# Kernel optimization log

Measured on AMD Instinct MI355X. Metric: run time of the kernel, lower is better.

The kernel has to match this reference:

```python
import jax, jax.numpy as jnp
import numpy as np

EPS = 1e-7
INF = 1e8
SOFT_CENTER_RADIUS = 3.0
TOPK = 13
IOU_WEIGHT = 3.0
NUM_CLASSES = 80
N_PRIORS = 33600
NUM_GT = 256
IMG = 1024.0


def setup_inputs() -> dict:
    key = jax.random.key(0)
    k1, k2, k3, k4, k5, k6, k7 = jax.random.split(key, 7)
    n, g, c = N_PRIORS, NUM_GT, NUM_CLASSES
    pred_scores = jax.random.normal(k1, (n, c), jnp.float32)
    # priors: (cx, cy, stride, stride)
    ctr = jax.random.uniform(k2, (n, 2), jnp.float32) * IMG
    stride = jnp.full((n, 1), 8.0, jnp.float32)
    priors = jnp.concatenate([ctr, stride, stride], axis=-1)
    # predicted boxes, x1y1x2y2
    pwh = jax.random.uniform(k3, (n, 2), jnp.float32) * 96.0 + 8.0
    pctr = jax.random.uniform(k4, (n, 2), jnp.float32) * IMG
    pred_bboxes = jnp.concatenate([pctr - pwh / 2, pctr + pwh / 2], axis=-1)
    # gt boxes, x1y1x2y2
    gwh = jax.random.uniform(k5, (g, 2), jnp.float32) * 192.0 + 16.0
    gctr = jax.random.uniform(k6, (g, 2), jnp.float32) * IMG
    gt_bboxes = jnp.concatenate([gctr - gwh / 2, gctr + gwh / 2], axis=-1)
    gt_labels = jax.random.randint(k7, (g,), 0, c, dtype=jnp.int32).astype(jnp.int64)
    return {"pred_scores": pred_scores, "priors": priors,
            "pred_bboxes": pred_bboxes, "gt_bboxes": gt_bboxes,
            "gt_labels": gt_labels}


def _pairwise_iou(a, b):
    # a: (n,4), b: (g,4), x1y1x2y2 -> (n,g)
    area_a = (a[:, 2] - a[:, 0]) * (a[:, 3] - a[:, 1])
    area_b = (b[:, 2] - b[:, 0]) * (b[:, 3] - b[:, 1])
    lt = jnp.maximum(a[:, None, :2], b[None, :, :2])
    rb = jnp.minimum(a[:, None, 2:], b[None, :, 2:])
    wh = jnp.clip(rb - lt, 0.0, None)
    inter = wh[..., 0] * wh[..., 1]
    union = area_a[:, None] + area_b[None, :] - inter
    return inter / jnp.maximum(union, 1e-6)


def reference(pred_scores, priors, pred_bboxes, gt_bboxes, gt_labels):
    n, g = pred_bboxes.shape[0], gt_bboxes.shape[0]
    gt_labels = gt_labels.astype(jnp.int32)

    # ---- find_inside_points (box_dim == 4) ----
    pts = priors[:, :2]                                   # (n,2)
    lt = pts[:, None, :] - gt_bboxes[None, :, :2]
    rb = gt_bboxes[None, :, 2:] - pts[:, None, :]
    is_in_gts = jnp.min(jnp.concatenate([lt, rb], -1), -1) > 0   # (n,g)
    pad_bbox_flag = gt_bboxes.sum(-1) > 0                        # (g,)
    is_in_gts = is_in_gts & pad_bbox_flag[None, :]
    valid_mask = jnp.any(is_in_gts, -1)                          # (n,)

    # ---- soft center prior ----
    gt_center = (gt_bboxes[:, :2] + gt_bboxes[:, 2:]) * 0.5      # (g,2)
    dist = jnp.sqrt(((pts[:, None, :] - gt_center[None, :, :]) ** 2).sum(-1))
    dist = dist / priors[:, 2:3]                                 # / stride
    dist = dist * valid_mask[:, None].astype(dist.dtype)
    soft_center_prior = jnp.power(10.0, dist - SOFT_CENTER_RADIUS)

    # ---- iou cost ----
    ious = _pairwise_iou(pred_bboxes, gt_bboxes)                 # (n,g)
    iou_cost = -jnp.log(ious + EPS) * IOU_WEIGHT

    # ---- soft classification cost (BCE-with-logits, iou targets) ----
    logits = pred_scores[:, gt_labels]                           # (n,g)
    scale = jnp.abs(ious - jax.nn.sigmoid(logits)) ** 2
    bce = jnp.maximum(logits, 0) - logits * ious + jnp.log1p(jnp.exp(-jnp.abs(logits)))
    cost = bce * scale + iou_cost + soft_center_prior
    cost = jnp.where(valid_mask[:, None], cost, INF)

    # ---- dynamic k matching (vectorized over GTs) ----
    K = min(TOPK, n)
    topk_ious, _ = jax.lax.top_k(ious.T, K)                      # (g,K)
    dynamic_ks = jnp.clip(topk_ious.sum(-1).astype(jnp.int32), 1, None)  # (g,)
    _, cand_idx = jax.lax.top_k(-cost.T, K)                      # (g,K) lowest-cost priors per gt
    sel = (jnp.arange(K)[None, :] < dynamic_ks[:, None]).astype(jnp.float32)
    matching = jnp.zeros((g, n), jnp.float32).at[
        jnp.arange(g)[:, None], cand_idx].set(sel).T             # (n,g)

    # resolve priors matched to multiple gts -> keep min-cost gt
    multi = matching.sum(-1) > 1
    onehot_min = jax.nn.one_hot(jnp.argmin(cost, -1), g, dtype=jnp.float32)
    matching = jnp.where(multi[:, None], onehot_min, matching)

    fg = matching.sum(-1) > 0
    matched_gt_inds = jnp.argmax(matching, -1)                   # (n,)
    matched_pred_ious = (matching * ious).sum(-1)                # (n,)

    final = fg & valid_mask
    assigned_gt_inds = jnp.where(final, matched_gt_inds + 1, 0)
    assigned_labels = jnp.where(final, gt_labels[matched_gt_inds], -1)
    max_overlaps = jnp.where(final, matched_pred_ious, -INF)
    return assigned_gt_inds, max_overlaps, assigned_labels
```

## Files before the change

kernel.cpp:

```cpp
#include <hip/hip_runtime.h>
#include <cstdint>

#define NPRI 33600
#define NGT  256
#define NCLS 80
#define KTOP 13
#define INF_F 1.0e8f
#define EPS_F 1e-7f
#define L10 3.3219280948873623f
#define SCN_T 512
#define NW   (SCN_T / 64)
#define CAPI 4096
#define CAPC 1024
#define RFIX 5.5f
#define NBX  32
#define NB   (NBX * NBX)
#define PREP_BLKS ((NPRI + 255) / 256)
#define NEGINF __int_as_float(0xff800000)

typedef unsigned long long u64;

__device__ __forceinline__ int get_label(const void* p, int j, int is64) {
    if (is64) return (int)((const long long*)p)[j];
    return ((const int*)p)[j];
}

__device__ __forceinline__ int bin1(float c) {
    int b = (int)floorf(c * 0.03125f);
    return b < 0 ? 0 : (b > NBX - 1 ? NBX - 1 : b);
}

__device__ __forceinline__ float wave_max_bc_f32(float v) {
    #pragma unroll
    for (int off = 32; off > 0; off >>= 1) v = fmaxf(v, __shfl_down(v, off, 64));
    return __int_as_float(__builtin_amdgcn_readfirstlane(__float_as_int(v)));
}
__device__ __forceinline__ u64 wave_min_bc_u64(u64 v) {
    #pragma unroll
    for (int off = 32; off > 0; off >>= 1) { u64 o = __shfl_down(v, off, 64); v = (o < v) ? o : v; }
    unsigned lo = (unsigned)__builtin_amdgcn_readfirstlane((int)(v & 0xffffffffull));
    unsigned hi = (unsigned)__builtin_amdgcn_readfirstlane((int)(v >> 32));
    return (((u64)hi) << 32) | lo;
}
// ... 23 lines not shown
        if (lane == 0) dst[r] = bm;
    }
}

__device__ __forceinline__ float iou_exact(float4 pb, float areap, float gx1, float gy1,
                                           float gx2, float gy2, float areag) {
    float iw = fmaxf(fminf(pb.z, gx2) - fmaxf(pb.x, gx1), 0.0f);
    float ih = fmaxf(fminf(pb.w, gy2) - fmaxf(pb.y, gy1), 0.0f);
    float inter = iw * ih;
    return inter / fmaxf(areap + areag - inter, 1e-6f);
}
__device__ __forceinline__ float cost_exact(float4 p2, float gcx, float gcy,
                                            float l, float iou) {
    float dx = p2.x - gcx, dy = p2.y - gcy;
    float dist = sqrtf(dx * dx + dy * dy) / p2.z;
    float soft = exp2f((dist - 3.0f) * L10);
    float sig = 1.0f / (1.0f + expf(-l));
    float dd = iou - sig;
    float bce = fmaxf(l, 0.0f) - l * iou + log1pf(expf(-fabsf(l)));
    float iouc = -logf(iou + EPS_F) * 3.0f;
    return bce * (dd * dd) + iouc + soft;
}

__global__ __launch_bounds__(256) void k_prep(
        const float* __restrict__ priors, const float* __restrict__ gt,
        const void* labels, const float* __restrict__ pboxes,
        float4* __restrict__ pbp,
        int* count, int* firstgt, int* flag,
        int* histI, int* histC, int* maxbuf) {
    __shared__ float4 gbox[NGT];
    __shared__ int    gpad[NGT];
    __shared__ int    bad;
    __shared__ int    lhI[NB];
    __shared__ int    lhC[NB];
    __shared__ int    lmax0, lmax1;
    const int tid = threadIdx.x;
    const int b = blockIdx.x;
    if (b == 0 && tid == 0) bad = 0;
    if (tid == 0) { lmax0 = 0; lmax1 = 0; }
    for (int t = tid; t < NB; t += 256) { lhI[t] = 0; lhC[t] = 0; }
    {
        float4 bx = ((const float4*)gt)[tid];
        gbox[tid] = bx;
        gpad[tid] = ((bx.x + bx.y + bx.z + bx.w) > 0.0f) ? 1 : 0;
    }
    __syncthreads();
    if (b == 0 && tid < 128) {
        long long v = ((const long long*)labels)[tid];
        if (v < 0 || v >= NCLS) atomicOr(&bad, 1);
    }
    int g = b * 256 + tid;
    if (g < NPRI) {
        count[g] = 0; firstgt[g] = NGT;
        float4 pr = ((const float4*)priors)[g];
        float px = pr.x, py = pr.y;
        int v = 0;
        for (int j = 0; j < NGT; ++j) {
            float4 bx = gbox[j];
            float m = fminf(fminf(px - bx.x, py - bx.y), fminf(bx.z - px, bx.w - py));
            if (m > 0.0f && gpad[j]) { v = 1; break; }
        }
        float rad = pr.z * RFIX;
        float w = v ? rad * rad * (1.0f + 1e-5f) : -1.0f;
        float4 pb = ((const float4*)pboxes)[g];
        pbp[2 * g]     = pb;
        pbp[2 * g + 1] = make_float4(px, py, pr.z, w);
        float pcx = (pb.x + pb.z) * 0.5f, pcy = (pb.y + pb.w) * 0.5f;
        atomicAdd(&lhI[bin1(pcy) * NBX + bin1(pcx)], 1);
        atomicAdd(&lhC[bin1(py) * NBX + bin1(px)], 1);
        float hw = fmaxf((pb.z - pb.x) * 0.5f, 0.0f);
        float hh = fmaxf((pb.w - pb.y) * 0.5f, 0.0f);
        atomicMax(&lmax0, __float_as_int(fmaxf(hw, hh)));
        if (v) atomicMax(&lmax1, __float_as_int(w));
    }
    __syncthreads();
    for (int t = tid; t < NB; t += 256) {
        int h = lhI[t]; if (h) atomicAdd(&histI[t], h);
        h = lhC[t];     if (h) atomicAdd(&histC[t], h);
    }
    if (tid == 0) {
        atomicMax(&maxbuf[0], lmax0);
        atomicMax(&maxbuf[1], lmax1);
    }
    if (b == 0) {
        if (tid == 0) *flag = bad ? 0 : 1;
    }
}

__global__ __launch_bounds__(NB) void k_bins(
        const int* __restrict__ histI, const int* __restrict__ histC,
        int* startI, int* startC, int* curI, int* curC) {
    __shared__ int sc[NB];
    const int t = threadIdx.x;
    int h = histI[t];
    sc[t] = h;
    __syncthreads();
    for (int off = 1; off < NB; off <<= 1) {
        int u = (t >= off) ? sc[t - off] : 0;
        __syncthreads();
        sc[t] += u;
        __syncthreads();
    }
    int excl = sc[t] - h;
    startI[t] = excl; curI[t] = excl;
    if (t == NB - 1) startI[NB] = sc[t];
    __syncthreads();
    h = histC[t];
    sc[t] = h;
    __syncthreads();
    for (int off = 1; off < NB; off <<= 1) {
        int u = (t >= off) ? sc[t - off] : 0;
        __syncthreads();
        sc[t] += u;
        __syncthreads();
    }
    excl = sc[t] - h;
    startC[t] = excl; curC[t] = excl;
    if (t == NB - 1) startC[NB] = sc[t];
}

__global__ __launch_bounds__(256) void k_scatter(
        const float4* __restrict__ pbp,
        int* curI, int* curC,
        float4* __restrict__ A_pb, float4* __restrict__ A_pc) {
    const int i = blockIdx.x * 256 + threadIdx.x;
    if (i >= NPRI) return;
    float4 pb = pbp[2 * i];
    float4 p2 = pbp[2 * i + 1];
    float pcx = (pb.x + pb.z) * 0.5f, pcy = (pb.y + pb.w) * 0.5f;
    int r = atomicAdd(&curI[bin1(pcy) * NBX + bin1(pcx)], 1);
    A_pb[r] = pb;
    int r2 = atomicAdd(&curC[bin1(p2.y) * NBX + bin1(p2.x)], 1);
    A_pc[r2] = make_float4(p2.x, p2.y, p2.w, __int_as_float(i));
}

__global__ __launch_bounds__(SCN_T) void k_scan(
        const float* __restrict__ scores,
        const float4* __restrict__ pbp,
        const float4* __restrict__ A_pb, const float4* __restrict__ A_pc,
        const int* __restrict__ startI, const int* __restrict__ startC,
        const int* __restrict__ maxbuf,
        const float* __restrict__ gt, const void* labels, const int* flag,
        int* count, int* firstgt) {
    const int tid = threadIdx.x, lane = tid & 63, wid = tid >> 6;
    const int j = blockIdx.x;
    const int is64 = *flag;

    const float4 gb = ((const float4*)gt)[j];
    const float gx1 = gb.x, gy1 = gb.y, gx2 = gb.z, gy2 = gb.w;
    const float areag = (gx2 - gx1) * (gy2 - gy1);
    const float gcx = (gx1 + gx2) * 0.5f, gcy = (gy1 + gy2) * 0.5f;
    const int lab = get_label(labels, j, is64);
    const float hmax = __int_as_float(maxbuf[0]);
    const float wmax = __int_as_float(maxbuf[1]);
    const float M = 2.0f * hmax + 1.0f;
    const float rmax = sqrtf(fmaxf(wmax, 0.0f)) + 1.0f;

    __shared__ int s_ni, s_nc, s_mode;
    __shared__ float s_dmax;
    __shared__ float liou[CAPI];
    __shared__ int lcost[CAPC];
    __shared__ float wiof[(NW - 1) * KTOP];
    __shared__ u64 wco[NW * KTOP];
    __shared__ u64 csel[KTOP];
    __shared__ float s_iou13[KTOP];
    if (tid == 0) { s_ni = 0; s_nc = 0; }
    __syncthreads();

    {
        int lox = bin1(gx1 - M), hix = bin1(gx2 + M);
        int loy = bin1(gy1 - M), hiy = bin1(gy2 + M);
        for (int by = loy; by <= hiy; ++by) {
            int s0 = startI[by * NBX + lox];
            int e0 = startI[by * NBX + hix + 1];
            for (int r = s0 + tid; r < e0; r += SCN_T) {
                float4 pb = A_pb[r];
                float areap = (pb.z - pb.x) * (pb.w - pb.y);
                float iou = iou_exact(pb, areap, gx1, gy1, gx2, gy2, areag);
                if (iou > 0.0f) {
                    int p = atomicAdd(&s_ni, 1);
                    if (p < CAPI) liou[p] = iou;
                }
            }
        }
    }
    {
        int lox = bin1(gcx - rmax), hix = bin1(gcx + rmax);
        int loy = bin1(gcy - rmax), hiy = bin1(gcy + rmax);
        for (int by = loy; by <= hiy; ++by) {
            int s0 = startC[by * NBX + lox];
            int e0 = startC[by * NBX + hix + 1];
            for (int r = s0 + tid; r < e0; r += SCN_T) {
                float4 pc = A_pc[r];
                float dx = pc.x - gcx, dy = pc.y - gcy;
                if (dx * dx + dy * dy <= pc.z) {
                    int p = atomicAdd(&s_nc, 1);
                    if (p < CAPC) lcost[p] = __float_as_int(pc.w);
                }
            }
        }
    }
    __syncthreads();
    const int ni = s_ni, nc = s_nc;
    const int ncc = (nc < CAPC) ? nc : CAPC;
    const bool fI = (ni > CAPI);

    if (wid == 0) {
        u64 lf[KTOP];
        #pragma unroll
        for (int s = 0; s < KTOP; ++s) lf[s] = ~0ull;
        for (int k = lane; k < ncc; k += 64) {
            int i = lcost[k];
            float4 pb = pbp[2 * i];
            float4 p2 = pbp[2 * i + 1];
            float areap = (pb.z - pb.x) * (pb.w - pb.y);
            float iou = iou_exact(pb, areap, gx1, gy1, gx2, gy2, areag);
            float ec = cost_exact(p2, gcx, gcy, scores[(size_t)i * NCLS + lab], iou);
            u64 ck = (((u64)__float_as_uint(ec)) << 32) | (unsigned)i;
            if (ck < lf[KTOP - 1]) {
                lf[KTOP - 1] = ck;
                #pragma unroll
                for (int s = KTOP - 1; s > 0; --s)
                    if (lf[s] < lf[s - 1]) { u64 t = lf[s]; lf[s] = lf[s - 1]; lf[s - 1] = t; }
            }
        }
        wave_merge_minN<KTOP>(lf, csel, lane);
        if (lane == 0) {
            u64 tk = csel[KTOP - 1];
            int mode; float dmax = 0.0f;
            if (tk == ~0ull) mode = 2;
            else {
                float tau = __uint_as_float((unsigned)(tk >> 32));
                if (!(tau < 9.0e7f)) mode = 2;
                else {
                    dmax = 3.0f + __log2f(tau + 1e-5f) * (1.0f / L10) + 4e-3f;
                    mode = (dmax > RFIX || nc > CAPC) ? 1 : 0;
                }
            }
            s_mode = mode; s_dmax = dmax;
        }
    } else if (!fI) {
        float lf[KTOP];
        #pragma unroll
        for (int s = 0; s < KTOP; ++s) lf[s] = NEGINF;
        int nn = (ni < CAPI) ? ni : CAPI;
        for (int k = (wid - 1) * 64 + lane; k < nn; k += 64 * (NW - 1)) {
            float v = liou[k];
            if (v > lf[0]) {
                lf[0] = v;
                #pragma unroll
                for (int s = 0; s < KTOP - 1; ++s)
                    if (lf[s] > lf[s + 1]) { float t = lf[s]; lf[s] = lf[s + 1]; lf[s + 1] = t; }
            }
        }
        wave_merge_max13_f32<KTOP>(lf, &wiof[(wid - 1) * KTOP], lane);
    }
    __syncthreads();

    if (fI) {
        if (wid > 0) {
            float lf[KTOP];
            #pragma unroll
            for (int s = 0; s < KTOP; ++s) lf[s] = NEGINF;
            for (int i = (wid - 1) * 64 + lane; i < NPRI; i += 64 * (NW - 1)) {
                float4 pb = pbp[2 * i];
                float areap = (pb.z - pb.x) * (pb.w - pb.y);
                float iou = iou_exact(pb, areap, gx1, gy1, gx2, gy2, areag);
                if (iou > 0.0f && iou > lf[0]) {
                    lf[0] = iou;
                    #pragma unroll
                    for (int s = 0; s < KTOP - 1; ++s)
                        if (lf[s] > lf[s + 1]) { float t = lf[s]; lf[s] = lf[s + 1]; lf[s + 1] = t; }
                }
            }
            wave_merge_max13_f32<KTOP>(lf, &wiof[(wid - 1) * KTOP], lane);
        }
        __syncthreads();
    }

    if (wid == 0) {
        int p = 0;
        for (int r = 0; r < KTOP; ++r) {
            float cur = (lane < NW - 1 && p < KTOP) ? wiof[lane * KTOP + p] : NEGINF;
            float bm = wave_max_bc_f32(cur);
            u64 m = __ballot(cur == bm && bm != NEGINF);
            int first = __ffsll(m) - 1;
            if (lane == first) p++;
            if (lane == 0) s_iou13[r] = bm;
        }
    }

    int mode = s_mode;
    if (mode == 1) {
        const float dmax = s_dmax;
        if (tid == 0) s_nc = 0;
        __syncthreads();
        for (int i = tid; i < NPRI; i += SCN_T) {
            float4 p2 = pbp[2 * i + 1];
            if (p2.w > 0.0f) {
                float dx = p2.x - gcx, dy = p2.y - gcy;
                float rad = p2.z * dmax;
                if (dx * dx + dy * dy <= rad * rad * (1.0f + 1e-5f)) {
                    int p = atomicAdd(&s_nc, 1);
                    if (p < CAPC) lcost[p] = i;
                }
            }
        }
        __syncthreads();
        int nc2 = s_nc;
        if (nc2 <= CAPC) {
            if (wid == 0) {
                u64 lf[KTOP];
                #pragma unroll
                for (int s = 0; s < KTOP; ++s) lf[s] = ~0ull;
                for (int k = lane; k < nc2; k += 64) {
                    int i = lcost[k];
                    float4 pb = pbp[2 * i];
                    float4 p2 = pbp[2 * i + 1];
                    float areap = (pb.z - pb.x) * (pb.w - pb.y);
                    float iou = iou_exact(pb, areap, gx1, gy1, gx2, gy2, areag);
                    float ec = cost_exact(p2, gcx, gcy, scores[(size_t)i * NCLS + lab], iou);
                    u64 ck = (((u64)__float_as_uint(ec)) << 32) | (unsigned)i;
                    if (ck < lf[KTOP - 1]) {
                        lf[KTOP - 1] = ck;
                        #pragma unroll
                        for (int s = KTOP - 1; s > 0; --s)
                            if (lf[s] < lf[s - 1]) { u64 t = lf[s]; lf[s] = lf[s - 1]; lf[s - 1] = t; }
                    }
                }
                wave_merge_minN<KTOP>(lf, csel, lane);
            }
        } else {
            mode = 2;
        }
        __syncthreads();
    }
    if (mode == 2) {
        u64 lf[KTOP];
        #pragma unroll
        for (int s = 0; s < KTOP; ++s) lf[s] = ~0ull;
        for (int i = tid; i < NPRI; i += SCN_T) {
            float4 pb = pbp[2 * i];
            float4 p2 = pbp[2 * i + 1];
            float areap = (pb.z - pb.x) * (pb.w - pb.y);
            float iou = iou_exact(pb, areap, gx1, gy1, gx2, gy2, areag);
            float ec = INF_F;
            if (p2.w > 0.0f) ec = cost_exact(p2, gcx, gcy, scores[(size_t)i * NCLS + lab], iou);
            u64 k2 = (((u64)__float_as_uint(ec)) << 32) | (unsigned)i;
            if (k2 < lf[KTOP - 1]) {
                lf[KTOP - 1] = k2;
                #pragma unroll
                for (int s = KTOP - 1; s > 0; --s)
                    if (lf[s] < lf[s - 1]) { u64 t = lf[s]; lf[s] = lf[s - 1]; lf[s - 1] = t; }
            }
        }
        wave_merge_minN<KTOP>(lf, &wco[wid * KTOP], lane);
        __syncthreads();
        if (wid == 0) {
            int p = 0;
            for (int r = 0; r < KTOP; ++r) {
                u64 cur = (lane < NW && p < KTOP) ? wco[lane * KTOP + p] : ~0ull;
                u64 bm = wave_min_bc_u64(cur);
                if (cur == bm && bm != ~0ull) p++;
                if (lane == 0) csel[r] = bm;
            }
        }
        __syncthreads();
    }

    __syncthreads();
    if (wid == 0) {
        float tsum = 0.0f;
        #pragma unroll
        for (int r = 0; r < KTOP; ++r) {
            float v = s_iou13[r];
            tsum += (v == NEGINF) ? 0.0f : v;
        }
        int ks = (int)tsum;
        if (ks < 1) ks = 1;
        if (lane < KTOP && lane < ks) {
            u64 mine = csel[lane];
            if (mine != ~0ull) {
                int idx = (int)(unsigned)(mine & 0xFFFFFFFFull);
                atomicAdd(&count[idx], 1);
                atomicMin(&firstgt[idx], j);
            }
        }
    }
}

__global__ __launch_bounds__(256) void k_assign(
        const float* __restrict__ scores,
        const float4* __restrict__ pbp, const float* __restrict__ gt,
        const void* labels, const int* flag,
        const int* __restrict__ count, const int* __restrict__ firstgt,
        float* __restrict__ out) {
    __shared__ float4 gbox[NGT];
    __shared__ int glab[NGT];
    __shared__ float gcxs[NGT], gcys[NGT], gareas[NGT];
    __shared__ int s_nm;
    __shared__ int s_mlist[256];
    __shared__ u64 red4[4];
    const int tid = threadIdx.x;
    const int is64 = *flag;
    {
        float4 b = ((const float4*)gt)[tid];
        gbox[tid] = b;
        glab[tid] = get_label(labels, tid, is64);
        gcxs[tid] = (b.x + b.z) * 0.5f;
        gcys[tid] = (b.y + b.w) * 0.5f;
        gareas[tid] = (b.z - b.x) * (b.w - b.y);
    }
    if (tid == 0) s_nm = 0;
    __syncthreads();
    const int i = blockIdx.x * 256 + tid;
    const bool act = (i < NPRI);
    if (act) {
        float4 p2 = pbp[2 * i + 1];
        int v = (p2.w > 0.0f) ? 1 : 0;
        int c = count[i];
        float o0 = 0.0f, o1 = -INF_F, o2 = -1.0f;
        if (v && c == 1) {
            int j = firstgt[i];
            float4 pb = pbp[2 * i];
            float areap = (pb.z - pb.x) * (pb.w - pb.y);
            float4 g = gbox[j];
            float iw = fmaxf(fminf(pb.z, g.z) - fmaxf(pb.x, g.x), 0.0f);
            float ih = fmaxf(fminf(pb.w, g.w) - fmaxf(pb.y, g.y), 0.0f);
            float inter = iw * ih;
            float iou = inter / fmaxf(areap + gareas[j] - inter, 1e-6f);
            o0 = (float)(j + 1); o1 = iou; o2 = (float)glab[j];
        } else if (v && c > 1) {
            int p = atomicAdd(&s_nm, 1);
            s_mlist[p] = i;
        }
        out[i] = o0;
        out[NPRI + i] = o1;
        out[2 * NPRI + i] = o2;
    }
    __syncthreads();
    const int nm = s_nm;
    const int j = tid;
    for (int m = 0; m < nm; ++m) {
        const int ii = s_mlist[m];
        float4 pb = pbp[2 * ii];
        float4 p2 = pbp[2 * ii + 1];
        float areap = (pb.z - pb.x) * (pb.w - pb.y);

        float4 g = gbox[j];
        float iw = fmaxf(fminf(pb.z, g.z) - fmaxf(pb.x, g.x), 0.0f);
        float ih = fmaxf(fminf(pb.w, g.w) - fmaxf(pb.y, g.y), 0.0f);
        float inter = iw * ih;
        float iou = inter / fmaxf(areap + gareas[j] - inter, 1e-6f);
        float dx = p2.x - gcxs[j], dy = p2.y - gcys[j];
        float dist = sqrtf(dx * dx + dy * dy) / p2.z;
        float soft = exp2f((dist - 3.0f) * L10);
        float l = scores[(size_t)ii * NCLS + glab[j]];
        float sig = 1.0f / (1.0f + expf(-l));
        float dd = iou - sig;
        float bce = fmaxf(l, 0.0f) - l * iou + log1pf(expf(-fabsf(l)));
        float cost = bce * (dd * dd) + (-logf(iou + EPS_F) * 3.0f) + soft;

        u64 key = (((u64)__float_as_uint(cost)) << 32) | (unsigned)j;
        u64 v = key;
        #pragma unroll
        for (int off = 32; off > 0; off >>= 1) {
            u64 o = __shfl_down(v, off, 64);
            v = (o < v) ? o : v;
        }
        if ((tid & 63) == 0) red4[tid >> 6] = v;
        __syncthreads();
        u64 best = red4[0];
        #pragma unroll
        for (int q = 1; q < 4; ++q) best = (red4[q] < best) ? red4[q] : best;
        if (key == best) {
            out[ii] = (float)(j + 1);
            out[NPRI + ii] = iou;
            out[2 * NPRI + ii] = (float)glab[j];
        }
        __syncthreads();
    }
}

extern "C" void kernel_launch(void* const* d_in, const int* in_sizes, int n_in,
                              void* d_out, int out_size, void* d_ws, size_t ws_size,
                              hipStream_t stream) {
    const float* scores = (const float*)d_in[0];
    const float* priors = (const float*)d_in[1];
    const float* pboxes = (const float*)d_in[2];
    const float* gt     = (const float*)d_in[3];
    const void*  labels = d_in[4];
    float* out = (float*)d_out;

    char* ws = (char*)d_ws;
    size_t off = 0;
    auto alloc = [&](size_t bytes) { size_t o = off; off = (off + bytes + 255) & ~(size_t)255; return o; };
    int*    flag    = (int*)(ws + alloc(4));
    int*    count   = (int*)(ws + alloc((size_t)NPRI * 4));
    int*    firstgt = (int*)(ws + alloc((size_t)NPRI * 4));
    int*    histI   = (int*)(ws + alloc((size_t)(2 * NB + 2) * 4));
    int*    histC   = histI + NB;
    int*    maxbuf  = histI + 2 * NB;
    int*    startI  = (int*)(ws + alloc((size_t)(NB + 1) * 4));
    int*    startC  = (int*)(ws + alloc((size_t)(NB + 1) * 4));
    int*    curI    = (int*)(ws + alloc((size_t)NB * 4));
    int*    curC    = (int*)(ws + alloc((size_t)NB * 4));
    float4* pbp     = (float4*)(ws + alloc((size_t)NPRI * 32));
    float4* A_pb    = (float4*)(ws + alloc((size_t)NPRI * 16));
    float4* A_pc    = (float4*)(ws + alloc((size_t)NPRI * 16));
    (void)ws_size;

    hipMemsetAsync(histI, 0, (size_t)(2 * NB + 2) * 4, stream);
    hipLaunchKernelGGL(k_prep, dim3(PREP_BLKS), dim3(256), 0, stream,
                       priors, gt, labels, pboxes, pbp, count, firstgt, flag,
                       histI, histC, maxbuf);
    hipLaunchKernelGGL(k_bins, dim3(1), dim3(NB), 0, stream,
                       histI, histC, startI, startC, curI, curC);
    hipLaunchKernelGGL(k_scatter, dim3(PREP_BLKS), dim3(256), 0, stream,
                       pbp, curI, curC, A_pb, A_pc);
    hipLaunchKernelGGL(k_scan, dim3(NGT), dim3(SCN_T), 0, stream,
                       scores, pbp, A_pb, A_pc, startI, startC, maxbuf,
                       gt, labels, flag, count, firstgt);
    hipLaunchKernelGGL(k_assign, dim3((NPRI + 255) / 256), dim3(256), 0, stream,
                       scores, pbp, gt, labels, flag, count, firstgt, out);
}
```

Before: 157.0 us.

## Fuse five-kernel pipeline into one cooperative kernel with grid syncs

Replaces the prep, bin-prefix, scatter, per-GT scan and assign kernels with a single cooperative kernel of 256 blocks of 512 threads, separated by grid.sync barriers. The inside-GT test is now done wave-wide with a ballot across 256 GT boxes instead of a serial loop per thread. This removes four kernel launch gaps. In exchange every phase runs on only 256 blocks, and the grid barriers plus higher shared memory use per block could limit occupancy.

```diff
diff --git a/kernel.cpp b/kernel.cpp
--- a/kernel.cpp
+++ b/kernel.cpp
@@ -1,4 +1,5 @@
 #include <hip/hip_runtime.h>
+#include <hip/hip_cooperative_groups.h>
 #include <cstdint>
 
 #define NPRI 33600
@@ -15,10 +16,10 @@
 #define RFIX 5.5f
 #define NBX  32
 #define NB   (NBX * NBX)
-#define PREP_BLKS ((NPRI + 255) / 256)
 #define NEGINF __int_as_float(0xff800000)
 
 typedef unsigned long long u64;
+namespace cg = cooperative_groups;
 
 __device__ __forceinline__ int get_label(const void* p, int j, int is64) {
     if (is64) return (int)((const long long*)p)[j];
@@ -88,140 +89,25 @@
     return bce * (dd * dd) + iouc + soft;
 }
 
-__global__ __launch_bounds__(256) void k_prep(
-        const float* __restrict__ priors, const float* __restrict__ gt,
-        const void* labels, const float* __restrict__ pboxes,
-        float4* __restrict__ pbp,
+__global__ __launch_bounds__(SCN_T) void k_all(
+        const float* __restrict__ scores, const float* __restrict__ priors,
+        const float* __restrict__ pboxes, const float* __restrict__ gt,
+        const void* labels,
+        float4* __restrict__ pbp, float4* __restrict__ A_pb, float4* __restrict__ A_pc,
+        int* histI, int* histC, int* maxbuf,
+        int* startI, int* startC, int* curI, int* curC,
         int* count, int* firstgt, int* flag,
-        int* histI, int* histC, int* maxbuf) {
+        float* __restrict__ out) {
+    cg::grid_group grid = cg::this_grid();
+    const int tid = threadIdx.x, lane = tid & 63, wid = tid >> 6;
+    const int bid = blockIdx.x;
+
     __shared__ float4 gbox[NGT];
     __shared__ int    gpad[NGT];
     __shared__ int    bad;
-    __shared__ int    lhI[NB];
-    __shared__ int    lhC[NB];
+    __shared__ int    lhI[NB], lhC[NB];
     __shared__ int    lmax0, lmax1;
-    const int tid = threadIdx.x;
-    const int b = blockIdx.x;
-    if (b == 0 && tid == 0) bad = 0;
-    if (tid == 0) { lmax0 = 0; lmax1 = 0; }
-    for (int t = tid; t < NB; t += 256) { lhI[t] = 0; lhC[t] = 0; }
-    {
-        float4 bx = ((const float4*)gt)[tid];
-        gbox[tid] = bx;
-        gpad[tid] = ((bx.x + bx.y + bx.z + bx.w) > 0.0f) ? 1 : 0;
-    }
-    __syncthreads();
-    if (b == 0 && tid < 128) {
-        long long v = ((const long long*)labels)[tid];
-        if (v < 0 || v >= NCLS) atomicOr(&bad, 1);
-    }
-    int g = b * 256 + tid;
-    if (g < NPRI) {
-        count[g] = 0; firstgt[g] = NGT;
-        float4 pr = ((const float4*)priors)[g];
-        float px = pr.x, py = pr.y;
-        int v = 0;
-        for (int j = 0; j < NGT; ++j) {
-            float4 bx = gbox[j];
-            float m = fminf(fminf(px - bx.x, py - bx.y), fminf(bx.z - px, bx.w - py));
-            if (m > 0.0f && gpad[j]) { v = 1; break; }
-        }
-        float rad = pr.z * RFIX;
-        float w = v ? rad * rad * (1.0f + 1e-5f) : -1.0f;
-        float4 pb = ((const float4*)pboxes)[g];
-        pbp[2 * g]     = pb;
-        pbp[2 * g + 1] = make_float4(px, py, pr.z, w);
-        float pcx = (pb.x + pb.z) * 0.5f, pcy = (pb.y + pb.w) * 0.5f;
-        atomicAdd(&lhI[bin1(pcy) * NBX + bin1(pcx)], 1);
-        atomicAdd(&lhC[bin1(py) * NBX + bin1(px)], 1);
-        float hw = fmaxf((pb.z - pb.x) * 0.5f, 0.0f);
-        float hh = fmaxf((pb.w - pb.y) * 0.5f, 0.0f);
-        atomicMax(&lmax0, __float_as_int(fmaxf(hw, hh)));
-        if (v) atomicMax(&lmax1, __float_as_int(w));
-    }
-    __syncthreads();
-    for (int t = tid; t < NB; t += 256) {
-        int h = lhI[t]; if (h) atomicAdd(&histI[t], h);
-        h = lhC[t];     if (h) atomicAdd(&histC[t], h);
-    }
-    if (tid == 0) {
-        atomicMax(&maxbuf[0], lmax0);
-        atomicMax(&maxbuf[1], lmax1);
-    }
-    if (b == 0) {
-        if (tid == 0) *flag = bad ? 0 : 1;
-    }
-}
-
-__global__ __launch_bounds__(NB) void k_bins(
-        const int* __restrict__ histI, const int* __restrict__ histC,
-        int* startI, int* startC, int* curI, int* curC) {
-    __shared__ int sc[NB];
-    const int t = threadIdx.x;
-    int h = histI[t];
-    sc[t] = h;
-    __syncthreads();
-    for (int off = 1; off < NB; off <<= 1) {
-        int u = (t >= off) ? sc[t - off] : 0;
-        __syncthreads();
-        sc[t] += u;
-        __syncthreads();
-    }
-    int excl = sc[t] - h;
-    startI[t] = excl; curI[t] = excl;
-    if (t == NB - 1) startI[NB] = sc[t];
-    __syncthreads();
-    h = histC[t];
-    sc[t] = h;
-    __syncthreads();
-    for (int off = 1; off < NB; off <<= 1) {
-        int u = (t >= off) ? sc[t - off] : 0;
-        __syncthreads();
-        sc[t] += u;
-        __syncthreads();
-    }
-    excl = sc[t] - h;
-    startC[t] = excl; curC[t] = excl;
-    if (t == NB - 1) startC[NB] = sc[t];
-}
-
-__global__ __launch_bounds__(256) void k_scatter(
-        const float4* __restrict__ pbp,
-        int* curI, int* curC,
-        float4* __restrict__ A_pb, float4* __restrict__ A_pc) {
-    const int i = blockIdx.x * 256 + threadIdx.x;
-    if (i >= NPRI) return;
-    float4 pb = pbp[2 * i];
-    float4 p2 = pbp[2 * i + 1];
-    float pcx = (pb.x + pb.z) * 0.5f, pcy = (pb.y + pb.w) * 0.5f;
-    int r = atomicAdd(&curI[bin1(pcy) * NBX + bin1(pcx)], 1);
-    A_pb[r] = pb;
-    int r2 = atomicAdd(&curC[bin1(p2.y) * NBX + bin1(p2.x)], 1);
-    A_pc[r2] = make_float4(p2.x, p2.y, p2.w, __int_as_float(i));
-}
-
-__global__ __launch_bounds__(SCN_T) void k_scan(
-        const float* __restrict__ scores,
-        const float4* __restrict__ pbp,
-        const float4* __restrict__ A_pb, const float4* __restrict__ A_pc,
-        const int* __restrict__ startI, const int* __restrict__ startC,
-        const int* __restrict__ maxbuf,
-        const float* __restrict__ gt, const void* labels, const int* flag,
-        int* count, int* firstgt) {
-    const int tid = threadIdx.x, lane = tid & 63, wid = tid >> 6;
-    const int j = blockIdx.x;
-    const int is64 = *flag;
-
-    const float4 gb = ((const float4*)gt)[j];
-    const float gx1 = gb.x, gy1 = gb.y, gx2 = gb.z, gy2 = gb.w;
-    const float areag = (gx2 - gx1) * (gy2 - gy1);
-    const float gcx = (gx1 + gx2) * 0.5f, gcy = (gy1 + gy2) * 0.5f;
-    const int lab = get_label(labels, j, is64);
-    const float hmax = __int_as_float(maxbuf[0]);
-    const float wmax = __int_as_float(maxbuf[1]);
-    const float M = 2.0f * hmax + 1.0f;
-    const float rmax = sqrtf(fmaxf(wmax, 0.0f)) + 1.0f;
-
+    __shared__ int    sc[512];
     __shared__ int s_ni, s_nc, s_mode;
     __shared__ float s_dmax;
     __shared__ float liou[CAPI];
@@ -230,110 +116,212 @@
     __shared__ u64 wco[NW * KTOP];
     __shared__ u64 csel[KTOP];
     __shared__ float s_iou13[KTOP];
-    if (tid == 0) { s_ni = 0; s_nc = 0; }
+    __shared__ int glab[NGT];
+    __shared__ float gcxs[NGT], gcys[NGT], gareas[NGT];
+    __shared__ int s_nm;
+    __shared__ int s_mlist[512];
+    __shared__ u64 red8[NW];
+
+    if (tid == 0) { bad = 0; lmax0 = 0; lmax1 = 0; }
+    if (tid < NGT) {
+        float4 bx = ((const float4*)gt)[tid];
+        gbox[tid] = bx;
+        gpad[tid] = ((bx.x + bx.y + bx.z + bx.w) > 0.0f) ? 1 : 0;
+    }
+    for (int t = tid; t < NB; t += SCN_T) { lhI[t] = 0; lhC[t] = 0; }
     __syncthreads();
-
+    if (bid == 0 && tid < 128) {
+        long long v = ((const long long*)labels)[tid];
+        if (v < 0 || v >= NCLS) atomicOr(&bad, 1);
+    }
     {
-        int lox = bin1(gx1 - M), hix = bin1(gx2 + M);
-        int loy = bin1(gy1 - M), hiy = bin1(gy2 + M);
-        for (int by = loy; by <= hiy; ++by) {
-            int s0 = startI[by * NBX + lox];
-            int e0 = startI[by * NBX + hix + 1];
-            for (int r = s0 + tid; r < e0; r += SCN_T) {
-                float4 pb = A_pb[r];
+        const int gw = bid * NW + wid;
+        for (int i = gw; i < NPRI; i += NGT * NW) {
+            float4 pr = ((const float4*)priors)[i];
+            float px = pr.x, py = pr.y;
+            bool hit = false;
+            #pragma unroll
+            for (int q = 0; q < 4; ++q) {
+                float4 bx = gbox[lane + 64 * q];
+                float m = fminf(fminf(px - bx.x, py - bx.y), fminf(bx.z - px, bx.w - py));
+                hit |= (m > 0.0f && gpad[lane + 64 * q]);
+            }
+            u64 msk = __ballot(hit);
+            if (lane == 0) {
+                int v = (msk != 0ull) ? 1 : 0;
+                float rad = pr.z * RFIX;
+                float w = v ? rad * rad * (1.0f + 1e-5f) : -1.0f;
+                float4 pb = ((const float4*)pboxes)[i];
+                pbp[2 * i]     = pb;
+                pbp[2 * i + 1] = make_float4(px, py, pr.z, w);
+                count[i] = 0; firstgt[i] = NGT;
+                float pcx = (pb.x + pb.z) * 0.5f, pcy = (pb.y + pb.w) * 0.5f;
+                atomicAdd(&lhI[bin1(pcy) * NBX + bin1(pcx)], 1);
+                atomicAdd(&lhC[bin1(py) * NBX + bin1(px)], 1);
+                float hw = fmaxf((pb.z - pb.x) * 0.5f, 0.0f);
+                float hh = fmaxf((pb.w - pb.y) * 0.5f, 0.0f);
+                atomicMax(&lmax0, __float_as_int(fmaxf(hw, hh)));
+                if (v) atomicMax(&lmax1, __float_as_int(w));
+            }
+        }
+    }
+    __syncthreads();
+    for (int t = tid; t < NB; t += SCN_T) {
+        int h = lhI[t]; if (h) atomicAdd(&histI[t], h);
+        h = lhC[t];     if (h) atomicAdd(&histC[t], h);
+    }
+    if (tid == 0) {
+        atomicMax(&maxbuf[0], lmax0);
+        atomicMax(&maxbuf[1], lmax1);
+        if (bid == 0) *flag = bad ? 0 : 1;
+    }
+    grid.sync();
+
+    const int is64 = *flag;
+
+    if (bid == 0) {
+        int h0 = histI[2 * tid], h1 = histI[2 * tid + 1];
+        int ps = h0 + h1;
+        sc[tid] = ps;
+        __syncthreads();
+        for (int off = 1; off < 512; off <<= 1) {
+            int u = (tid >= off) ? sc[tid - off] : 0;
+            __syncthreads();
+            sc[tid] += u;
+            __syncthreads();
+        }
+        int e0 = sc[tid] - ps;
+        startI[2 * tid] = e0;          curI[2 * tid] = e0;
+        startI[2 * tid + 1] = e0 + h0; curI[2 * tid + 1] = e0 + h0;
+        if (tid == 511) startI[NB] = sc[tid];
+        __syncthreads();
+        h0 = histC[2 * tid]; h1 = histC[2 * tid + 1];
+        ps = h0 + h1;
+        sc[tid] = ps;
+        __syncthreads();
+        for (int off = 1; off < 512; off <<= 1) {
+            int u = (tid >= off) ? sc[tid - off] : 0;
+            __syncthreads();
+            sc[tid] += u;
+            __syncthreads();
+        }
+        e0 = sc[tid] - ps;
+        startC[2 * tid] = e0;          curC[2 * tid] = e0;
+        startC[2 * tid + 1] = e0 + h0; curC[2 * tid + 1] = e0 + h0;
+        if (tid == 511) startC[NB] = sc[tid];
+    }
+    grid.sync();
+
+    {
+        int i = bid * SCN_T + tid;
+        if (i < NPRI) {
+            float4 pb = pbp[2 * i];
+            float4 p2 = pbp[2 * i + 1];
+            float pcx = (pb.x + pb.z) * 0.5f, pcy = (pb.y + pb.w) * 0.5f;
+            int r = atomicAdd(&curI[bin1(pcy) * NBX + bin1(pcx)], 1);
+            A_pb[r] = pb;
+            int r2 = atomicAdd(&curC[bin1(p2.y) * NBX + bin1(p2.x)], 1);
+            A_pc[r2] = make_float4(p2.x, p2.y, p2.w, __int_as_float(i));
+        }
+    }
+    grid.sync();
+
+    {
+        const int j = bid;
+        const float4 gb = gbox[j];
+        const float gx1 = gb.x, gy1 = gb.y, gx2 = gb.z, gy2 = gb.w;
+        const float areag = (gx2 - gx1) * (gy2 - gy1);
+        const float gcx = (gx1 + gx2) * 0.5f, gcy = (gy1 + gy2) * 0.5f;
+        const int lab = get_label(labels, j, is64);
+        const float hmax = __int_as_float(maxbuf[0]);
+        const float wmax = __int_as_float(maxbuf[1]);
+        const float M = 2.0f * hmax + 1.0f;
+        const float rmax = sqrtf(fmaxf(wmax, 0.0f)) + 1.0f;
+
+        if (tid == 0) { s_ni = 0; s_nc = 0; }
+        __syncthreads();
+
+        {
+            int lox = bin1(gx1 - M), hix = bin1(gx2 + M);
+            int loy = bin1(gy1 - M), hiy = bin1(gy2 + M);
+            for (int by = loy; by <= hiy; ++by) {
+                int s0 = startI[by * NBX + lox];
+                int e0 = startI[by * NBX + hix + 1];
+                for (int r = s0 + tid; r < e0; r += SCN_T) {
+                    float4 pb = A_pb[r];
+                    float areap = (pb.z - pb.x) * (pb.w - pb.y);
+                    float iou = iou_exact(pb, areap, gx1, gy1, gx2, gy2, areag);
+                    if (iou > 0.0f) {
+                        int p = atomicAdd(&s_ni, 1);
+                        if (p < CAPI) liou[p] = iou;
+                    }
+                }
+            }
+        }
+        {
+            int lox = bin1(gcx - rmax), hix = bin1(gcx + rmax);
+            int loy = bin1(gcy - rmax), hiy = bin1(gcy + rmax);
+            for (int by = loy; by <= hiy; ++by) {
+                int s0 = startC[by * NBX + lox];
+                int e0 = startC[by * NBX + hix + 1];
+                for (int r = s0 + tid; r < e0; r += SCN_T) {
+                    float4 pc = A_pc[r];
+                    float dx = pc.x - gcx, dy = pc.y - gcy;
+                    if (dx * dx + dy * dy <= pc.z) {
+                        int p = atomicAdd(&s_nc, 1);
+                        if (p < CAPC) lcost[p] = __float_as_int(pc.w);
+                    }
+                }
+            }
+        }
+        __syncthreads();
+        const int ni = s_ni, nc = s_nc;
+        const int ncc = (nc < CAPC) ? nc : CAPC;
+        const bool fI = (ni > CAPI);
+
+        if (wid == 0) {
+            u64 lf[KTOP];
+            #pragma unroll
+            for (int s = 0; s < KTOP; ++s) lf[s] = ~0ull;
+            for (int k = lane; k < ncc; k += 64) {
+                int i = lcost[k];
+                float4 pb = pbp[2 * i];
+                float4 p2 = pbp[2 * i + 1];
                 float areap = (pb.z - pb.x) * (pb.w - pb.y);
                 float iou = iou_exact(pb, areap, gx1, gy1, gx2, gy2, areag);
-                if (iou > 0.0f) {
-                    int p = atomicAdd(&s_ni, 1);
-                    if (p < CAPI) liou[p] = iou;
-                }
-            }
-        }
-    }
-    {
-        int lox = bin1(gcx - rmax), hix = bin1(gcx + rmax);
-        int loy = bin1(gcy - rmax), hiy = bin1(gcy + rmax);
-        for (int by = loy; by <= hiy; ++by) {
-            int s0 = startC[by * NBX + lox];
-            int e0 = startC[by * NBX + hix + 1];
-            for (int r = s0 + tid; r < e0; r += SCN_T) {
-                float4 pc = A_pc[r];
-                float dx = pc.x - gcx, dy = pc.y - gcy;
-                if (dx * dx + dy * dy <= pc.z) {
-                    int p = atomicAdd(&s_nc, 1);
-                    if (p < CAPC) lcost[p] = __float_as_int(pc.w);
-                }
-            }
-        }
-    }
-    __syncthreads();
-    const int ni = s_ni, nc = s_nc;
-    const int ncc = (nc < CAPC) ? nc : CAPC;
-    const bool fI = (ni > CAPI);
-
-    if (wid == 0) {
-        u64 lf[KTOP];
-        #pragma unroll
-        for (int s = 0; s < KTOP; ++s) lf[s] = ~0ull;
-        for (int k = lane; k < ncc; k += 64) {
-            int i = lcost[k];
-            float4 pb = pbp[2 * i];
-            float4 p2 = pbp[2 * i + 1];
-            float areap = (pb.z - pb.x) * (pb.w - pb.y);
-            float iou = iou_exact(pb, areap, gx1, gy1, gx2, gy2, areag);
-            float ec = cost_exact(p2, gcx, gcy, scores[(size_t)i * NCLS + lab], iou);
-            u64 ck = (((u64)__float_as_uint(ec)) << 32) | (unsigned)i;
-            if (ck < lf[KTOP - 1]) {
-                lf[KTOP - 1] = ck;
-                #pragma unroll
-                for (int s = KTOP - 1; s > 0; --s)
-                    if (lf[s] < lf[s - 1]) { u64 t = lf[s]; lf[s] = lf[s - 1]; lf[s - 1] = t; }
-            }
-        }
-        wave_merge_minN<KTOP>(lf, csel, lane);
-        if (lane == 0) {
-            u64 tk = csel[KTOP - 1];
-            int mode; float dmax = 0.0f;
-            if (tk == ~0ull) mode = 2;
-            else {
-                float tau = __uint_as_float((unsigned)(tk >> 32));
-                if (!(tau < 9.0e7f)) mode = 2;
+                float ec = cost_exact(p2, gcx, gcy, scores[(size_t)i * NCLS + lab], iou);
+                u64 ck = (((u64)__float_as_uint(ec)) << 32) | (unsigned)i;
+                if (ck < lf[KTOP - 1]) {
+                    lf[KTOP - 1] = ck;
+                    #pragma unroll
+                    for (int s = KTOP - 1; s > 0; --s)
+                        if (lf[s] < lf[s - 1]) { u64 t = lf[s]; lf[s] = lf[s - 1]; lf[s - 1] = t; }
+                }
+            }
+            wave_merge_minN<KTOP>(lf, csel, lane);
+            if (lane == 0) {
+                u64 tk = csel[KTOP - 1];
+                int mode; float dmax = 0.0f;
+                if (tk == ~0ull) mode = 2;
                 else {
-                    dmax = 3.0f + __log2f(tau + 1e-5f) * (1.0f / L10) + 4e-3f;
-                    mode = (dmax > RFIX || nc > CAPC) ? 1 : 0;
-                }
-            }
-            s_mode = mode; s_dmax = dmax;
-        }
-    } else if (!fI) {
-        float lf[KTOP];
-        #pragma unroll
-        for (int s = 0; s < KTOP; ++s) lf[s] = NEGINF;
-        int nn = (ni < CAPI) ? ni : CAPI;
-        for (int k = (wid - 1) * 64 + lane; k < nn; k += 64 * (NW - 1)) {
-            float v = liou[k];
-            if (v > lf[0]) {
-                lf[0] = v;
-                #pragma unroll
-                for (int s = 0; s < KTOP - 1; ++s)
-                    if (lf[s] > lf[s + 1]) { float t = lf[s]; lf[s] = lf[s + 1]; lf[s + 1] = t; }
-            }
-        }
-        wave_merge_max13_f32<KTOP>(lf, &wiof[(wid - 1) * KTOP], lane);
-    }
-    __syncthreads();
-
-    if (fI) {
-        if (wid > 0) {
+                    float tau = __uint_as_float((unsigned)(tk >> 32));
+                    if (!(tau < 9.0e7f)) mode = 2;
+                    else {
+                        dmax = 3.0f + __log2f(tau + 1e-5f) * (1.0f / L10) + 4e-3f;
+                        mode = (dmax > RFIX || nc > CAPC) ? 1 : 0;
+                    }
+                }
+                s_mode = mode; s_dmax = dmax;
+            }
+        } else if (!fI) {
             float lf[KTOP];
             #pragma unroll
             for (int s = 0; s < KTOP; ++s) lf[s] = NEGINF;
-            for (int i = (wid - 1) * 64 + lane; i < NPRI; i += 64 * (NW - 1)) {
-                float4 pb = pbp[2 * i];
-                float areap = (pb.z - pb.x) * (pb.w - pb.y);
-                float iou = iou_exact(pb, areap, gx1, gy1, gx2, gy2, areag);
-                if (iou > 0.0f && iou > lf[0]) {
-                    lf[0] = iou;
+            int nn = (ni < CAPI) ? ni : CAPI;
+            for (int k = (wid - 1) * 64 + lane; k < nn; k += 64 * (NW - 1)) {
+                float v = liou[k];
+                if (v > lf[0]) {
+                    lf[0] = v;
                     #pragma unroll
                     for (int s = 0; s < KTOP - 1; ++s)
                         if (lf[s] > lf[s + 1]) { float t = lf[s]; lf[s] = lf[s + 1]; lf[s + 1] = t; }
@@ -342,209 +330,218 @@
             wave_merge_max13_f32<KTOP>(lf, &wiof[(wid - 1) * KTOP], lane);
         }
         __syncthreads();
-    }
-
-    if (wid == 0) {
-        int p = 0;
-        for (int r = 0; r < KTOP; ++r) {
-            float cur = (lane < NW - 1 && p < KTOP) ? wiof[lane * KTOP + p] : NEGINF;
-            float bm = wave_max_bc_f32(cur);
-            u64 m = __ballot(cur == bm && bm != NEGINF);
-            int first = __ffsll(m) - 1;
-            if (lane == first) p++;
-            if (lane == 0) s_iou13[r] = bm;
-        }
-    }
-
-    int mode = s_mode;
-    if (mode == 1) {
-        const float dmax = s_dmax;
-        if (tid == 0) s_nc = 0;
-        __syncthreads();
-        for (int i = tid; i < NPRI; i += SCN_T) {
-            float4 p2 = pbp[2 * i + 1];
-            if (p2.w > 0.0f) {
-                float dx = p2.x - gcx, dy = p2.y - gcy;
-                float rad = p2.z * dmax;
-                if (dx * dx + dy * dy <= rad * rad * (1.0f + 1e-5f)) {
-                    int p = atomicAdd(&s_nc, 1);
-                    if (p < CAPC) lcost[p] = i;
-                }
-            }
-        }
-        __syncthreads();
-        int nc2 = s_nc;
-        if (nc2 <= CAPC) {
-            if (wid == 0) {
-                u64 lf[KTOP];
+
+        if (fI) {
+            if (wid > 0) {
+                float lf[KTOP];
                 #pragma unroll
-                for (int s = 0; s < KTOP; ++s) lf[s] = ~0ull;
-                for (int k = lane; k < nc2; k += 64) {
-                    int i = lcost[k];
+                for (int s = 0; s < KTOP; ++s) lf[s] = NEGINF;
+                for (int i = (wid - 1) * 64 + lane; i < NPRI; i += 64 * (NW - 1)) {
                     float4 pb = pbp[2 * i];
-                    float4 p2 = pbp[2 * i + 1];
                     float areap = (pb.z - pb.x) * (pb.w - pb.y);
                     float iou = iou_exact(pb, areap, gx1, gy1, gx2, gy2, areag);
-                    float ec = cost_exact(p2, gcx, gcy, scores[(size_t)i * NCLS + lab], iou);
-                    u64 ck = (((u64)__float_as_uint(ec)) << 32) | (unsigned)i;
-                    if (ck < lf[KTOP - 1]) {
-                        lf[KTOP - 1] = ck;
+                    if (iou > 0.0f && iou > lf[0]) {
+                        lf[0] = iou;
                         #pragma unroll
-                        for (int s = KTOP - 1; s > 0; --s)
-                            if (lf[s] < lf[s - 1]) { u64 t = lf[s]; lf[s] = lf[s - 1]; lf[s - 1] = t; }
+                        for (int s = 0; s < KTOP - 1; ++s)
+                            if (lf[s] > lf[s + 1]) { float t = lf[s]; lf[s] = lf[s + 1]; lf[s + 1] = t; }
                     }
                 }
-                wave_merge_minN<KTOP>(lf, csel, lane);
-            }
-        } else {
-            mode = 2;
-        }
-        __syncthreads();
-    }
-    if (mode == 2) {
-        u64 lf[KTOP];
-        #pragma unroll
-        for (int s = 0; s < KTOP; ++s) lf[s] = ~0ull;
-        for (int i = tid; i < NPRI; i += SCN_T) {
-            float4 pb = pbp[2 * i];
-            float4 p2 = pbp[2 * i + 1];
-            float areap = (pb.z - pb.x) * (pb.w - pb.y);
-            float iou = iou_exact(pb, areap, gx1, gy1, gx2, gy2, areag);
-            float ec = INF_F;
-            if (p2.w > 0.0f) ec = cost_exact(p2, gcx, gcy, scores[(size_t)i * NCLS + lab], iou);
-            u64 k2 = (((u64)__float_as_uint(ec)) << 32) | (unsigned)i;
-            if (k2 < lf[KTOP - 1]) {
-                lf[KTOP - 1] = k2;
-                #pragma unroll
-                for (int s = KTOP - 1; s > 0; --s)
-                    if (lf[s] < lf[s - 1]) { u64 t = lf[s]; lf[s] = lf[s - 1]; lf[s - 1] = t; }
-            }
-        }
-        wave_merge_minN<KTOP>(lf, &wco[wid * KTOP], lane);
-        __syncthreads();
+                wave_merge_max13_f32<KTOP>(lf, &wiof[(wid - 1) * KTOP], lane);
+            }
+            __syncthreads();
+        }
+
         if (wid == 0) {
             int p = 0;
             for (int r = 0; r < KTOP; ++r) {
-                u64 cur = (lane < NW && p < KTOP) ? wco[lane * KTOP + p] : ~0ull;
-                u64 bm = wave_min_bc_u64(cur);
-                if (cur == bm && bm != ~0ull) p++;
-                if (lane == 0) csel[r] = bm;
-            }
-        }
-        __syncthreads();
-    }
-
-    __syncthreads();
-    if (wid == 0) {
-        float tsum = 0.0f;
-        #pragma unroll
-        for (int r = 0; r < KTOP; ++r) {
-            float v = s_iou13[r];
-            tsum += (v == NEGINF) ? 0.0f : v;
-        }
-        int ks = (int)tsum;
-        if (ks < 1) ks = 1;
-        if (lane < KTOP && lane < ks) {
-            u64 mine = csel[lane];
-            if (mine != ~0ull) {
-                int idx = (int)(unsigned)(mine & 0xFFFFFFFFull);
-                atomicAdd(&count[idx], 1);
-                atomicMin(&firstgt[idx], j);
-            }
-        }
-    }
-}
-
-__global__ __launch_bounds__(256) void k_assign(
-        const float* __restrict__ scores,
-        const float4* __restrict__ pbp, const float* __restrict__ gt,
-        const void* labels, const int* flag,
-        const int* __restrict__ count, const int* __restrict__ firstgt,
-        float* __restrict__ out) {
-    __shared__ float4 gbox[NGT];
-    __shared__ int glab[NGT];
-    __shared__ float gcxs[NGT], gcys[NGT], gareas[NGT];
-    __shared__ int s_nm;
-    __shared__ int s_mlist[256];
-    __shared__ u64 red4[4];
-    const int tid = threadIdx.x;
-    const int is64 = *flag;
+                float cur = (lane < NW - 1 && p < KTOP) ? wiof[lane * KTOP + p] : NEGINF;
+                float bm = wave_max_bc_f32(cur);
+                u64 m = __ballot(cur == bm && bm != NEGINF);
+                int first = __ffsll(m) - 1;
+                if (lane == first) p++;
+                if (lane == 0) s_iou13[r] = bm;
+            }
+        }
+
+        int mode = s_mode;
+        if (mode == 1) {
+            const float dmax = s_dmax;
+            if (tid == 0) s_nc = 0;
+            __syncthreads();
+            for (int i = tid; i < NPRI; i += SCN_T) {
+                float4 p2 = pbp[2 * i + 1];
+                if (p2.w > 0.0f) {
+                    float dx = p2.x - gcx, dy = p2.y - gcy;
+                    float rad = p2.z * dmax;
+                    if (dx * dx + dy * dy <= rad * rad * (1.0f + 1e-5f)) {
+                        int p = atomicAdd(&s_nc, 1);
+                        if (p < CAPC) lcost[p] = i;
+                    }
+                }
+            }
+            __syncthreads();
+            int nc2 = s_nc;
+            if (nc2 <= CAPC) {
+                if (wid == 0) {
+                    u64 lf[KTOP];
+                    #pragma unroll
+                    for (int s = 0; s < KTOP; ++s) lf[s] = ~0ull;
+                    for (int k = lane; k < nc2; k += 64) {
+                        int i = lcost[k];
+                        float4 pb = pbp[2 * i];
+                        float4 p2 = pbp[2 * i + 1];
+                        float areap = (pb.z - pb.x) * (pb.w - pb.y);
+                        float iou = iou_exact(pb, areap, gx1, gy1, gx2, gy2, areag);
+                        float ec = cost_exact(p2, gcx, gcy, scores[(size_t)i * NCLS + lab], iou);
+                        u64 ck = (((u64)__float_as_uint(ec)) << 32) | (unsigned)i;
+                        if (ck < lf[KTOP - 1]) {
+                            lf[KTOP - 1] = ck;
+                            #pragma unroll
+                            for (int s = KTOP - 1; s > 0; --s)
+                                if (lf[s] < lf[s - 1]) { u64 t = lf[s]; lf[s] = lf[s - 1]; lf[s - 1] = t; }
+                        }
+                    }
+                    wave_merge_minN<KTOP>(lf, csel, lane);
+                }
+            } else {
+                mode = 2;
+            }
+            __syncthreads();
+        }
+        if (mode == 2) {
+            u64 lf[KTOP];
+            #pragma unroll
+            for (int s = 0; s < KTOP; ++s) lf[s] = ~0ull;
+            for (int i = tid; i < NPRI; i += SCN_T) {
+                float4 pb = pbp[2 * i];
+                float4 p2 = pbp[2 * i + 1];
+                float areap = (pb.z - pb.x) * (pb.w - pb.y);
+                float iou = iou_exact(pb, areap, gx1, gy1, gx2, gy2, areag);
+                float ec = INF_F;
+                if (p2.w > 0.0f) ec = cost_exact(p2, gcx, gcy, scores[(size_t)i * NCLS + lab], iou);
+                u64 k2 = (((u64)__float_as_uint(ec)) << 32) | (unsigned)i;
+                if (k2 < lf[KTOP - 1]) {
+                    lf[KTOP - 1] = k2;
+                    #pragma unroll
+                    for (int s = KTOP - 1; s > 0; --s)
+                        if (lf[s] < lf[s - 1]) { u64 t = lf[s]; lf[s] = lf[s - 1]; lf[s - 1] = t; }
+                }
+            }
+            wave_merge_minN<KTOP>(lf, &wco[wid * KTOP], lane);
+            __syncthreads();
+            if (wid == 0) {
+                int p = 0;
+                for (int r = 0; r < KTOP; ++r) {
+                    u64 cur = (lane < NW && p < KTOP) ? wco[lane * KTOP + p] : ~0ull;
+                    u64 bm = wave_min_bc_u64(cur);
+                    if (cur == bm && bm != ~0ull) p++;
+                    if (lane == 0) csel[r] = bm;
+                }
+            }
+            __syncthreads();
+        }
+
+        __syncthreads();
+        if (wid == 0) {
+            float tsum = 0.0f;
+            #pragma unroll
+            for (int r = 0; r < KTOP; ++r) {
+                float v = s_iou13[r];
+                tsum += (v == NEGINF) ? 0.0f : v;
+            }
+            int ks = (int)tsum;
+            if (ks < 1) ks = 1;
+            if (lane < KTOP && lane < ks) {
+                u64 mine = csel[lane];
+                if (mine != ~0ull) {
+                    int idx = (int)(unsigned)(mine & 0xFFFFFFFFull);
+                    atomicAdd(&count[idx], 1);
+                    atomicMin(&firstgt[idx], j);
+                }
+            }
+        }
+    }
+    grid.sync();
+
     {
-        float4 b = ((const float4*)gt)[tid];
-        gbox[tid] = b;
-        glab[tid] = get_label(labels, tid, is64);
-        gcxs[tid] = (b.x + b.z) * 0.5f;
-        gcys[tid] = (b.y + b.w) * 0.5f;
-        gareas[tid] = (b.z - b.x) * (b.w - b.y);
-    }
-    if (tid == 0) s_nm = 0;
-    __syncthreads();
-    const int i = blockIdx.x * 256 + tid;
-    const bool act = (i < NPRI);
-    if (act) {
-        float4 p2 = pbp[2 * i + 1];
-        int v = (p2.w > 0.0f) ? 1 : 0;
-        int c = count[i];
-        float o0 = 0.0f, o1 = -INF_F, o2 = -1.0f;
-        if (v && c == 1) {
-            int j = firstgt[i];
-            float4 pb = pbp[2 * i];
-            float areap = (pb.z - pb.x) * (pb.w - pb.y);
-            float4 g = gbox[j];
-            float iw = fmaxf(fminf(pb.z, g.z) - fmaxf(pb.x, g.x), 0.0f);
-            float ih = fmaxf(fminf(pb.w, g.w) - fmaxf(pb.y, g.y), 0.0f);
-            float inter = iw * ih;
-            float iou = inter / fmaxf(areap + gareas[j] - inter, 1e-6f);
-            o0 = (float)(j + 1); o1 = iou; o2 = (float)glab[j];
-        } else if (v && c > 1) {
-            int p = atomicAdd(&s_nm, 1);
-            s_mlist[p] = i;
-        }
-        out[i] = o0;
-        out[NPRI + i] = o1;
-        out[2 * NPRI + i] = o2;
-    }
-    __syncthreads();
-    const int nm = s_nm;
-    const int j = tid;
-    for (int m = 0; m < nm; ++m) {
-        const int ii = s_mlist[m];
-        float4 pb = pbp[2 * ii];
-        float4 p2 = pbp[2 * ii + 1];
-        float areap = (pb.z - pb.x) * (pb.w - pb.y);
-
-        float4 g = gbox[j];
-        float iw = fmaxf(fminf(pb.z, g.z) - fmaxf(pb.x, g.x), 0.0f);
-        float ih = fmaxf(fminf(pb.w, g.w) - fmaxf(pb.y, g.y), 0.0f);
-        float inter = iw * ih;
-        float iou = inter / fmaxf(areap + gareas[j] - inter, 1e-6f);
-        float dx = p2.x - gcxs[j], dy = p2.y - gcys[j];
-        float dist = sqrtf(dx * dx + dy * dy) / p2.z;
-        float soft = exp2f((dist - 3.0f) * L10);
-        float l = scores[(size_t)ii * NCLS + glab[j]];
-        float sig = 1.0f / (1.0f + expf(-l));
-        float dd = iou - sig;
-        float bce = fmaxf(l, 0.0f) - l * iou + log1pf(expf(-fabsf(l)));
-        float cost = bce * (dd * dd) + (-logf(iou + EPS_F) * 3.0f) + soft;
-
-        u64 key = (((u64)__float_as_uint(cost)) << 32) | (unsigned)j;
-        u64 v = key;
-        #pragma unroll
-        for (int off = 32; off > 0; off >>= 1) {
-            u64 o = __shfl_down(v, off, 64);
-            v = (o < v) ? o : v;
-        }
-        if ((tid & 63) == 0) red4[tid >> 6] = v;
-        __syncthreads();
-        u64 best = red4[0];
-        #pragma unroll
-        for (int q = 1; q < 4; ++q) best = (red4[q] < best) ? red4[q] : best;
-        if (key == best) {
-            out[ii] = (float)(j + 1);
-            out[NPRI + ii] = iou;
-            out[2 * NPRI + ii] = (float)glab[j];
-        }
-        __syncthreads();
+        if (tid < NGT) {
+            float4 b = gbox[tid];
+            glab[tid] = get_label(labels, tid, is64);
+            gcxs[tid] = (b.x + b.z) * 0.5f;
+            gcys[tid] = (b.y + b.w) * 0.5f;
+            gareas[tid] = (b.z - b.x) * (b.w - b.y);
+        }
+        if (tid == 0) s_nm = 0;
+        __syncthreads();
+        const int ia = bid * SCN_T + tid;
+        if (ia < NPRI) {
+            float4 p2 = pbp[2 * ia + 1];
+            int v = (p2.w > 0.0f) ? 1 : 0;
+            int c = count[ia];
+            float o0 = 0.0f, o1 = -INF_F, o2 = -1.0f;
+            if (v && c == 1) {
+                int j1 = firstgt[ia];
+                float4 pb = pbp[2 * ia];
+                float areap = (pb.z - pb.x) * (pb.w - pb.y);
+                float4 g = gbox[j1];
+                float iw = fmaxf(fminf(pb.z, g.z) - fmaxf(pb.x, g.x), 0.0f);
+                float ih = fmaxf(fminf(pb.w, g.w) - fmaxf(pb.y, g.y), 0.0f);
+                float inter = iw * ih;
+                float iou = inter / fmaxf(areap + gareas[j1] - inter, 1e-6f);
+                o0 = (float)(j1 + 1); o1 = iou; o2 = (float)glab[j1];
+            } else if (v && c > 1) {
+                int p = atomicAdd(&s_nm, 1);
+                s_mlist[p] = ia;
+            }
+            out[ia] = o0;
+            out[NPRI + ia] = o1;
+            out[2 * NPRI + ia] = o2;
+        }
+        __syncthreads();
+        const int nm = s_nm;
+        for (int m = 0; m < nm; ++m) {
+            const int ii = s_mlist[m];
+            u64 key = ~0ull;
+            float iouk = 0.0f;
+            if (tid < NGT) {
+                float4 pb = pbp[2 * ii];
+                float4 p2 = pbp[2 * ii + 1];
+                float areap = (pb.z - pb.x) * (pb.w - pb.y);
+                float4 g = gbox[tid];
+                float iw = fmaxf(fminf(pb.z, g.z) - fmaxf(pb.x, g.x), 0.0f);
+                float ih = fmaxf(fminf(pb.w, g.w) - fmaxf(pb.y, g.y), 0.0f);
+                float inter = iw * ih;
+                float iou = inter / fmaxf(areap + gareas[tid] - inter, 1e-6f);
+                float dx = p2.x - gcxs[tid], dy = p2.y - gcys[tid];
+                float dist = sqrtf(dx * dx + dy * dy) / p2.z;
+                float soft = exp2f((dist - 3.0f) * L10);
+                float l = scores[(size_t)ii * NCLS + glab[tid]];
+                float sig = 1.0f / (1.0f + expf(-l));
+                float dd = iou - sig;
+                float bce = fmaxf(l, 0.0f) - l * iou + log1pf(expf(-fabsf(l)));
+                float cost = bce * (dd * dd) + (-logf(iou + EPS_F) * 3.0f) + soft;
+                key = (((u64)__float_as_uint(cost)) << 32) | (unsigned)tid;
+                iouk = iou;
+            }
+            u64 v = key;
+            #pragma unroll
+            for (int off = 32; off > 0; off >>= 1) {
+                u64 o = __shfl_down(v, off, 64);
+                v = (o < v) ? o : v;
+            }
+            if (lane == 0) red8[wid] = v;
+            __syncthreads();
+            u64 best = red8[0];
+            #pragma unroll
+            for (int q = 1; q < NW; ++q) best = (red8[q] < best) ? red8[q] : best;
+            if (key == best && key != ~0ull) {
+                out[ii] = (float)(tid + 1);
+                out[NPRI + ii] = iouk;
+                out[2 * NPRI + ii] = (float)glab[tid];
+            }
+            __syncthreads();
+        }
     }
 }
 
@@ -577,16 +574,15 @@
     (void)ws_size;
 
     hipMemsetAsync(histI, 0, (size_t)(2 * NB + 2) * 4, stream);
-    hipLaunchKernelGGL(k_prep, dim3(PREP_BLKS), dim3(256), 0, stream,
-                       priors, gt, labels, pboxes, pbp, count, firstgt, flag,
-                       histI, histC, maxbuf);
-    hipLaunchKernelGGL(k_bins, dim3(1), dim3(NB), 0, stream,
-                       histI, histC, startI, startC, curI, curC);
-    hipLaunchKernelGGL(k_scatter, dim3(PREP_BLKS), dim3(256), 0, stream,
-                       pbp, curI, curC, A_pb, A_pc);
-    hipLaunchKernelGGL(k_scan, dim3(NGT), dim3(SCN_T), 0, stream,
-                       scores, pbp, A_pb, A_pc, startI, startC, maxbuf,
-                       gt, labels, flag, count, firstgt);
-    hipLaunchKernelGGL(k_assign, dim3((NPRI + 255) / 256), dim3(256), 0, stream,
-                       scores, pbp, gt, labels, flag, count, firstgt, out);
-}
+
+    void* args[] = {
+        (void*)&scores, (void*)&priors, (void*)&pboxes, (void*)&gt, (void*)&labels,
+        (void*)&pbp, (void*)&A_pb, (void*)&A_pc,
+        (void*)&histI, (void*)&histC, (void*)&maxbuf,
+        (void*)&startI, (void*)&startC, (void*)&curI, (void*)&curC,
+        (void*)&count, (void*)&firstgt, (void*)&flag,
+        (void*)&out
+    };
+    hipLaunchCooperativeKernel((const void*)k_all, dim3(NGT), dim3(SCN_T),
+                               args, 0, stream);
+}
```

New measurement: 251.6 us. 1.6x slower.
